# Kernel optimization log

Measured on AMD Instinct MI355X. Metric: run time of the kernel, lower is better.

## Reference

```python
import jax, jax.numpy as jnp
import numpy as np

NUM_HEADS = 16
WINDOW = 256


def setup_inputs() -> dict:
    key = jax.random.key(0)
    ks = jax.random.split(key, 9)
    B, S, E = 2, 2048, 1024
    sc = 1.0 / np.sqrt(E)
    return {
        "x": jax.random.normal(ks[0], (B, S, E), dtype=jnp.float32),
        "Wq": jax.random.normal(ks[1], (E, E), dtype=jnp.float32) * sc,
        "bq": jnp.zeros((E,), dtype=jnp.float32),
        "Wk": jax.random.normal(ks[2], (E, E), dtype=jnp.float32) * sc,
        "bk": jnp.zeros((E,), dtype=jnp.float32),
        "Wv": jax.random.normal(ks[3], (E, E), dtype=jnp.float32) * sc,
        "bv": jnp.zeros((E,), dtype=jnp.float32),
        "Wo": jax.random.normal(ks[4], (E, E), dtype=jnp.float32) * sc,
        "bo": jnp.zeros((E,), dtype=jnp.float32),
    }


def reference(x, Wq, bq, Wk, bk, Wv, bv, Wo, bo):
    B, S, E = x.shape
    H = NUM_HEADS
    D = E // H
    Q = (x @ Wq + bq).reshape(B, S, H, D).transpose(0, 2, 1, 3)  # [B,H,S,D]
    # Faithful to original: K is view(B, H, S, D), NOT a permute of (B,S,H,D)
    K = (x @ Wk + bk).reshape(B, H, S, D)
    V = (x @ Wv + bv).reshape(B, S, H, D).transpose(0, 2, 1, 3)  # [B,H,S,D]
    scores = jnp.einsum('bhqd,bhkd->bhqk', Q, K) / jnp.sqrt(jnp.float32(D))
    # sliding-window mask: j in [i-W, i+W)  (diag included, i+W exclusive)
    i = jnp.arange(S)[:, None]
    j = jnp.arange(S)[None, :]
    mask = (j >= i - WINDOW) & (j < i + WINDOW)  # [S,S]
    scores = jnp.where(mask, scores, -jnp.inf)
    attn = jax.nn.softmax(scores, axis=-1)
    out = jnp.einsum('bhqk,bhkd->bhqd', attn, V)  # [B,H,S,D]
    out = out.transpose(0, 2, 1, 3).reshape(B, S, E)
    return out @ Wo + bo
```

## Files before the change

kernel.cpp:

```cpp
#include <hip/hip_runtime.h>

#define S_LEN 2048
#define EMB   1024
#define HEADS 16
#define HDIM  64
#define WIN   256

typedef unsigned short u16;
typedef unsigned int   u32;
typedef float  f32x4  __attribute__((ext_vector_type(4)));
typedef __bf16 bf16x8 __attribute__((ext_vector_type(8)));
typedef unsigned short u16x4 __attribute__((ext_vector_type(4)));

typedef const __attribute__((address_space(1))) u32* gas_ptr;
typedef __attribute__((address_space(3))) u32*       las_ptr;

__device__ __forceinline__ void gload16(const void* g, void* l) {
    __builtin_amdgcn_global_load_lds((gas_ptr)g, (las_ptr)l, 16, 0, 0);
}

__device__ __forceinline__ u16 f2bf(float v) {
    u32 x = __builtin_bit_cast(u32, v);
    return (u16)((x + 0x7fffu + ((x >> 16) & 1u)) >> 16);
}
__device__ __forceinline__ u32 cvt_pk_bf16(float lo, float hi) {
    u32 r;
    asm volatile("v_cvt_pk_bf16_f32 %0, %1, %2" : "=v"(r) : "v"(lo), "v"(hi));
    return r;
}

__global__ __launch_bounds__(256)
void prep_kernel(const float* __restrict__ W0, const float* __restrict__ W1,
                 const float* __restrict__ W2, const float* __restrict__ W3,
                 u16* __restrict__ T0, u16* __restrict__ T1,
                 u16* __restrict__ T2, u16* __restrict__ T3,
                 const float* __restrict__ x, u16* __restrict__ xh, int n4)
{
    const int z = blockIdx.z;
    const int tid = threadIdx.x;

    if (z == 4) {
        int bid = blockIdx.x + 16 * blockIdx.y;
        for (int i = bid * 256 + tid; i < n4; i += 65536) {
            float4 v = reinterpret_cast<const float4*>(x)[i];
            u16x4 o;
            o[0] = f2bf(v.x); o[1] = f2bf(v.y); o[2] = f2bf(v.z); o[3] = f2bf(v.w);
            reinterpret_cast<u16x4*>(xh)[i] = o;
        }
        return;
    }

    const float* W = (z == 0) ? W0 : (z == 1) ? W1 : (z == 2) ? W2 : W3;
    u16* T = (z == 0) ? T0 : (z == 1) ? T1 : (z == 2) ? T2 : T3;

    __shared__ float Ts[64][68];
    const int k0 = blockIdx.x * 64, n0 = blockIdx.y * 64;

    int r = tid >> 2, c0 = (tid & 3) * 16;
#pragma unroll
    for (int q = 0; q < 4; ++q) {
        float4 v = *reinterpret_cast<const float4*>(W + (size_t)(k0 + r) * EMB + n0 + c0 + 4 * q);
        *reinterpret_cast<float4*>(&Ts[r][c0 + 4 * q]) = v;
    }
    __syncthreads();

    int n = tid >> 2, kk0 = (tid & 3) * 16;
    u16 hb[16];
#pragma unroll
    for (int e = 0; e < 16; ++e) hb[e] = f2bf(Ts[kk0 + e][n]);
    size_t base = (size_t)(n0 + n) * EMB + k0 + kk0;
#pragma unroll
    for (int q = 0; q < 2; ++q) {
        u32 w[4];
#pragma unroll
        for (int e = 0; e < 4; ++e)
            w[e] = (u32)hb[q * 8 + 2 * e] | ((u32)hb[q * 8 + 2 * e + 1] << 16);
        *reinterpret_cast<uint4*>(T + base + q * 8) = make_uint4(w[0], w[1], w[2], w[3]);
    }
}

template<int NFN, bool OUTBF>
__global__ __launch_bounds__(256, 3)
void mfma_gemm(const u16* __restrict__ A,
               const u16* __restrict__ B0, const u16* __restrict__ B1,
               const u16* __restrict__ B2,
               const float* __restrict__ bias0, const float* __restrict__ bias1,
               const float* __restrict__ bias2,
               float s0, float s1, float s2,
               void* __restrict__ Y0, void* __restrict__ Y1, void* __restrict__ Y2,
               int M, int N, int K)
{
    constexpr int TNB = NFN * 32;

    const int z = blockIdx.z;
    const u16*   Bt   = (z == 0) ? B0 : (z == 1) ? B1 : B2;
    const float* bias = (z == 0) ? bias0 : (z == 1) ? bias1 : bias2;
    const float  scl  = (z == 0) ? s0 : (z == 1) ? s1 : s2;
    void*        Y    = (z == 0) ? Y0 : (z == 1) ? Y1 : Y2;

    __shared__ u16 lds[(128 + TNB) * 32];
    u16* lA = lds;
    u16* lB = lds + 128 * 32;

    const int tid  = threadIdx.x;
    const int wid  = tid >> 6, lane = tid & 63;
    const int wr   = wid >> 1, wc = wid & 1;
    const int lr   = lane & 15, lg = lane >> 4;
    const int bm   = blockIdx.y * 128, bn = blockIdx.x * TNB;

    const int srow = lane >> 2;
    const int scol = (lane & 3) * 8;

    f32x4 acc[4][NFN];
#pragma unroll
    for (int i = 0; i < 4; ++i)
#pragma unroll
        for (int j = 0; j < NFN; ++j) acc[i][j] = (f32x4)0.0f;

    for (int k0 = 0; k0 < K; k0 += 32) {
#pragma unroll
        for (int q = 0; q < 2; ++q) {
            int ch = wid + q * 4;
            gload16(A + (size_t)(bm + ch * 16 + srow) * K + k0 + scol,
                    lA + ch * 512);
        }
#pragma unroll
        for (int q = 0; q < TNB / 64; ++q) {
            int ch = wid + q * 4;
            gload16(Bt + (size_t)(bn + ch * 16 + srow) * K + k0 + scol,
                    lB + ch * 512);
        }
        __syncthreads();

        bf16x8 a0[4], b0[NFN];
#pragma unroll
        for (int mf = 0; mf < 4; ++mf)
            a0[mf] = *reinterpret_cast<const bf16x8*>(
                lA + (wr * 64 + mf * 16 + lr) * 32 + lg * 8);
#pragma unroll
        for (int nf = 0; nf < NFN; ++nf)
            b0[nf] = *reinterpret_cast<const bf16x8*>(
                lB + (wc * NFN * 16 + nf * 16 + lr) * 32 + lg * 8);
#pragma unroll
        for (int mf = 0; mf < 4; ++mf)
#pragma unroll
            for (int nf = 0; nf < NFN; ++nf)
                acc[mf][nf] = __builtin_amdgcn_mfma_f32_16x16x32_bf16(
                    a0[mf], b0[nf], acc[mf][nf], 0, 0, 0);
        __syncthreads();
    }

#pragma unroll
    for (int nf = 0; nf < NFN; ++nf) {
        int col = bn + wc * NFN * 16 + nf * 16 + lr;
        float bs = bias[col];
#pragma unroll
        for (int mf = 0; mf < 4; ++mf) {
#pragma unroll
            for (int r = 0; r < 4; ++r) {
                int row = bm + wr * 64 + mf * 16 + lg * 4 + r;
                float val = (acc[mf][nf][r] + bs) * scl;
                if (OUTBF)
                    ((u16*)Y)[(size_t)row * N + col] = f2bf(val);
                else
                    ((float*)Y)[(size_t)row * N + col] = val;
            }
        }
    }
}

__global__ __launch_bounds__(512, 4)
void attn_mfma_kernel(const u16* __restrict__ Qb, const u16* __restrict__ Kb,
                      const u16* __restrict__ Vb, u16* __restrict__ AOh)
{
    __shared__ u16 Ks[64 * 64];
    __shared__ u16 Vt[64 * 64];
    __shared__ u16 Ps[8 * 16 * 64];

    constexpr float L2E = 1.44269504f;

    const int nwg = gridDim.x * gridDim.y * gridDim.z;
    int n  = blockIdx.x + gridDim.x * (blockIdx.y + gridDim.y * blockIdx.z);
    int sw = (n & 7) * (nwg >> 3) + (n >> 3);
    const int qb = sw & 15;
    const int h  = (sw >> 4) & 15;
    const int b  = sw >> 8;

    const int i0  = qb * 128;
    const int tid = threadIdx.x;
    const int wid = tid >> 6, lane = tid & 63;
    const int lr  = lane & 15, lg = lane >> 4;
    const int l7  = lr & 7;

    const u16* Kh = Kb + (size_t)b * S_LEN * EMB + (size_t)h * S_LEN * HDIM;

    bf16x8 qa[2];
    {
        const u16* qp = Qb + ((size_t)(b * S_LEN + i0 + wid * 16 + lr)) * EMB
                        + h * HDIM + lg * 8;
        qa[0] = *reinterpret_cast<const bf16x8*>(qp);
        qa[1] = *reinterpret_cast<const bf16x8*>(qp + 32);
    }

    float m2 = -1e30f, l = 0.0f;
    f32x4 o[4];
#pragma unroll
    for (int nf = 0; nf < 4; ++nf) o[nf] = (f32x4)0.0f;

    const int tlo = (2 * qb < 4) ? 0 : 2 * qb - 4;
    const int thi = (2 * qb + 5 > 31) ? 31 : 2 * qb + 5;
    const int qg  = i0 + wid * 16 + lr;

    const int kj   = lane >> 3;
    const int kgsw = (lane & 7) ^ kj;

    for (int t = tlo; t <= thi; ++t) {
        __syncthreads();

        gload16(Kh + (size_t)(t * 64 + wid * 8 + kj) * HDIM + kgsw * 8,
                Ks + wid * 512);

        {
            int jp = (tid & 31) * 2, dc = tid >> 5;
            const u16* vp = Vb + ((size_t)(b * S_LEN + t * 64 + jp)) * EMB
                            + h * HDIM + dc * 4;
            uint2 r0 = *reinterpret_cast<const uint2*>(vp);
            uint2 r1 = *reinterpret_cast<const uint2*>(vp + EMB);
            const u16* e0 = reinterpret_cast<const u16*>(&r0);
            const u16* e1 = reinterpret_cast<const u16*>(&r1);
            int jg = jp >> 3, jl = jp & 7;
#pragma unroll
            for (int e = 0; e < 4; ++e) {
                int d = dc * 4 + e;
                u32 w = (u32)e0[e] | ((u32)e1[e] << 16);
                *reinterpret_cast<u32*>(Vt + d * 64 + ((jg ^ (d & 7)) << 3) + jl) = w;
            }
        }
        __syncthreads();

        f32x4 s[4];
#pragma unroll
        for (int nf = 0; nf < 4; ++nf) s[nf] = (f32x4)0.0f;
#pragma unroll
        for (int ks = 0; ks < 2; ++ks) {
            int cg = (ks * 4 + lg) ^ l7;
#pragma unroll
            for (int nf = 0; nf < 4; ++nf) {
                bf16x8 kf = *reinterpret_cast<const bf16x8*>(
                    Ks + (nf * 16 + lr) * 64 + (cg << 3));
                s[nf] = __builtin_amdgcn_mfma_f32_16x16x32_bf16(kf, qa[ks], s[nf], 0, 0, 0);
            }
        }

        if (t <= 2 * qb - 3 || t >= 2 * qb + 4) {
            int klo = qg - WIN, khi = qg + WIN;
#pragma unroll
            for (int nf = 0; nf < 4; ++nf) {
#pragma unroll
                for (int r = 0; r < 4; ++r) {
                    int kg = t * 64 + nf * 16 + lg * 4 + r;
                    bool ok = (kg >= klo) && (kg < khi);
                    s[nf][r] = ok ? s[nf][r] : -1e30f;
                }
            }
        }

        float tmax = s[0][0];
#pragma unroll
        for (int nf = 0; nf < 4; ++nf)
#pragma unroll
            for (int r = 0; r < 4; ++r) tmax = fmaxf(tmax, s[nf][r]);
        tmax = fmaxf(tmax, __shfl_xor(tmax, 16));
        tmax = fmaxf(tmax, __shfl_xor(tmax, 32));
        float tmax2 = tmax * L2E;

        bool need = tmax2 > m2 + 12.0f;
        if (__any(need)) {
            float mn2 = fmaxf(m2, tmax2);
            float sc = __builtin_amdgcn_exp2f(m2 - mn2);
            m2 = mn2;
            l *= sc;
#pragma unroll
            for (int r = 0; r < 4; ++r) {
                float scr = __shfl(sc, lg * 4 + r);
#pragma unroll
                for (int nf = 0; nf < 4; ++nf) o[nf][r] *= scr;
            }
        }

        float ps = 0.0f;
#pragma unroll
        for (int nf = 0; nf < 4; ++nf) {
            float p0 = __builtin_amdgcn_exp2f(fmaf(s[nf][0], L2E, -m2));
            float p1 = __builtin_amdgcn_exp2f(fmaf(s[nf][1], L2E, -m2));
            float p2 = __builtin_amdgcn_exp2f(fmaf(s[nf][2], L2E, -m2));
            float p3 = __builtin_amdgcn_exp2f(fmaf(s[nf][3], L2E, -m2));
            ps += (p0 + p1) + (p2 + p3);
            u32 pk0 = cvt_pk_bf16(p0, p1);
            u32 pk1 = cvt_pk_bf16(p2, p3);
            int idx16 = wid * 1024 + lr * 64 +
                        (((nf * 2 + (lg >> 1)) ^ l7) << 3) + (lg & 1) * 4;
            *reinterpret_cast<uint2*>(Ps + idx16) = make_uint2(pk0, pk1);
        }
        ps += __shfl_xor(ps, 16);
        ps += __shfl_xor(ps, 32);
        l += ps;

#pragma unroll
        for (int ks = 0; ks < 2; ++ks) {
            int cg = (ks * 4 + lg) ^ l7;
            bf16x8 pf = *reinterpret_cast<const bf16x8*>(
                Ps + wid * 1024 + lr * 64 + (cg << 3));
#pragma unroll
            for (int nf = 0; nf < 4; ++nf) {
                bf16x8 vf = *reinterpret_cast<const bf16x8*>(
                    Vt + (nf * 16 + lr) * 64 + (cg << 3));
                o[nf] = __builtin_amdgcn_mfma_f32_16x16x32_bf16(pf, vf, o[nf], 0, 0, 0);
            }
        }
    }

    float inv = 1.0f / l;
#pragma unroll
    for (int r = 0; r < 4; ++r) {
        float invr = __shfl(inv, lg * 4 + r);
#pragma unroll
        for (int nf = 0; nf < 4; ++nf) {
            size_t idx = ((size_t)(b * S_LEN + i0 + wid * 16 + lg * 4 + r)) * EMB
                         + h * HDIM + nf * 16 + lr;
            AOh[idx] = f2bf(o[nf][r] * invr);
        }
    }
}

extern "C" void kernel_launch(void* const* d_in, const int* in_sizes, int n_in,
                              void* d_out, int out_size, void* d_ws, size_t ws_size,
                              hipStream_t stream)
{
    (void)n_in; (void)out_size; (void)ws_size;
    const float* x  = (const float*)d_in[0];
    const float* Wq = (const float*)d_in[1];
    const float* bq = (const float*)d_in[2];
    const float* Wk = (const float*)d_in[3];
    const float* bk = (const float*)d_in[4];
    const float* Wv = (const float*)d_in[5];
    const float* bv = (const float*)d_in[6];
    const float* Wo = (const float*)d_in[7];
    const float* bo = (const float*)d_in[8];
    float* out = (float*)d_out;

    const int B = in_sizes[0] / (S_LEN * EMB);
    const int M = B * S_LEN;

    u16* xh  = (u16*)d_ws;
    u16* WtQ = xh  + (size_t)M * EMB;
    u16* WtK = WtQ + (size_t)EMB * EMB;
    u16* WtV = WtK + (size_t)EMB * EMB;
    u16* WtO = WtV + (size_t)EMB * EMB;
    u16* Qb  = WtO + (size_t)EMB * EMB;
    u16* Kb  = Qb + (size_t)M * EMB;
    u16* Vb  = Kb + (size_t)M * EMB;
    u16* AOh = Vb + (size_t)M * EMB;

    int n4 = M * EMB / 4;
    dim3 gt(EMB / 64, EMB / 64, 5);
    prep_kernel<<<gt, 256, 0, stream>>>(Wq, Wk, Wv, Wo, WtQ, WtK, WtV, WtO,
                                        x, xh, n4);

    dim3 g1(EMB / 128, M / 128, 3);
    mfma_gemm<4, true><<<g1, 256, 0, stream>>>(
        xh, WtQ, WtK, WtV, bq, bk, bv, 0.125f, 1.0f, 1.0f,
        Qb, Kb, Vb, M, EMB, EMB);

    dim3 g2(S_LEN / 128, HEADS, B);
    attn_mfma_kernel<<<g2, 512, 0, stream>>>(Qb, Kb, Vb, AOh);

    dim3 g3(EMB / 64, M / 128, 1);
    mfma_gemm<2, false><<<g3, 256, 0, stream>>>(
        AOh, WtO, WtO, WtO, bo, bo, bo, 1.0f, 1.0f, 1.0f,
        out, out, out, M, EMB, EMB);
}
```

Measured before the change: 93.49 us.

## Double-buffer attention K/V tiles and deepen GEMM K-step with swizzled LDS

The attention kernel now keeps two LDS buffers for K and V. It prefetches the next tile's K (async global-to-LDS) and V (into registers) while computing on the current tile, which cuts the barriers per iteration from two to one and hides global load latency. The projection GEMM moves from a K-step of 32 to 64, using an XOR-swizzled LDS layout so the wider rows are read without bank conflicts. This halves the loop iterations and barriers. In exchange, LDS use in both kernels roughly doubles, which may reduce occupancy, and more registers are held across the iteration.

```diff
diff --git a/kernel.cpp b/kernel.cpp
--- a/kernel.cpp
+++ b/kernel.cpp
@@ -98,18 +98,19 @@
     const float  scl  = (z == 0) ? s0 : (z == 1) ? s1 : s2;
     void*        Y    = (z == 0) ? Y0 : (z == 1) ? Y1 : Y2;
 
-    __shared__ u16 lds[(128 + TNB) * 32];
+    __shared__ u16 lds[(128 + TNB) * 64];
     u16* lA = lds;
-    u16* lB = lds + 128 * 32;
+    u16* lB = lds + 128 * 64;
 
     const int tid  = threadIdx.x;
     const int wid  = tid >> 6, lane = tid & 63;
     const int wr   = wid >> 1, wc = wid & 1;
     const int lr   = lane & 15, lg = lane >> 4;
+    const int l7   = lr & 7;
     const int bm   = blockIdx.y * 128, bn = blockIdx.x * TNB;
 
-    const int srow = lane >> 2;
-    const int scol = (lane & 3) * 8;
+    const int crow = lane >> 3;
+    const int cgrp = (lane & 7) ^ crow;
 
     f32x4 acc[4][NFN];
 #pragma unroll
@@ -117,36 +118,40 @@
 #pragma unroll
         for (int j = 0; j < NFN; ++j) acc[i][j] = (f32x4)0.0f;
 
-    for (int k0 = 0; k0 < K; k0 += 32) {
-#pragma unroll
-        for (int q = 0; q < 2; ++q) {
-            int ch = wid + q * 4;
-            gload16(A + (size_t)(bm + ch * 16 + srow) * K + k0 + scol,
+    for (int k0 = 0; k0 < K; k0 += 64) {
+#pragma unroll
+        for (int q = 0; q < 4; ++q) {
+            int ch = wid * 4 + q;
+            gload16(A + (size_t)(bm + ch * 8 + crow) * K + k0 + cgrp * 8,
                     lA + ch * 512);
         }
 #pragma unroll
-        for (int q = 0; q < TNB / 64; ++q) {
-            int ch = wid + q * 4;
-            gload16(Bt + (size_t)(bn + ch * 16 + srow) * K + k0 + scol,
+        for (int q = 0; q < TNB / 32; ++q) {
+            int ch = wid * (TNB / 32) + q;
+            gload16(Bt + (size_t)(bn + ch * 8 + crow) * K + k0 + cgrp * 8,
                     lB + ch * 512);
         }
         __syncthreads();
 
-        bf16x8 a0[4], b0[NFN];
-#pragma unroll
-        for (int mf = 0; mf < 4; ++mf)
-            a0[mf] = *reinterpret_cast<const bf16x8*>(
-                lA + (wr * 64 + mf * 16 + lr) * 32 + lg * 8);
-#pragma unroll
-        for (int nf = 0; nf < NFN; ++nf)
-            b0[nf] = *reinterpret_cast<const bf16x8*>(
-                lB + (wc * NFN * 16 + nf * 16 + lr) * 32 + lg * 8);
-#pragma unroll
-        for (int mf = 0; mf < 4; ++mf)
+#pragma unroll
+        for (int ks = 0; ks < 2; ++ks) {
+            const int gsw = ((ks * 4 + lg) ^ l7) << 3;
+            bf16x8 a0[4], b0[NFN];
+#pragma unroll
+            for (int mf = 0; mf < 4; ++mf)
+                a0[mf] = *reinterpret_cast<const bf16x8*>(
+                    lA + (wr * 64 + mf * 16 + lr) * 64 + gsw);
 #pragma unroll
             for (int nf = 0; nf < NFN; ++nf)
-                acc[mf][nf] = __builtin_amdgcn_mfma_f32_16x16x32_bf16(
-                    a0[mf], b0[nf], acc[mf][nf], 0, 0, 0);
+                b0[nf] = *reinterpret_cast<const bf16x8*>(
+                    lB + (wc * NFN * 16 + nf * 16 + lr) * 64 + gsw);
+#pragma unroll
+            for (int mf = 0; mf < 4; ++mf)
+#pragma unroll
+                for (int nf = 0; nf < NFN; ++nf)
+                    acc[mf][nf] = __builtin_amdgcn_mfma_f32_16x16x32_bf16(
+                        a0[mf], b0[nf], acc[mf][nf], 0, 0, 0);
+        }
         __syncthreads();
     }
 
@@ -173,8 +178,8 @@
 void attn_mfma_kernel(const u16* __restrict__ Qb, const u16* __restrict__ Kb,
                       const u16* __restrict__ Vb, u16* __restrict__ AOh)
 {
-    __shared__ u16 Ks[64 * 64];
-    __shared__ u16 Vt[64 * 64];
+    __shared__ u16 Ks[2][64 * 64];
+    __shared__ u16 Vt[2][64 * 64];
     __shared__ u16 Ps[8 * 16 * 64];
 
     constexpr float L2E = 1.44269504f;
@@ -214,29 +219,35 @@
     const int kj   = lane >> 3;
     const int kgsw = (lane & 7) ^ kj;
 
+    const int vjp = (tid & 31) * 2, vdc = tid >> 5;
+    const u16* Vh = Vb + (size_t)b * S_LEN * EMB + h * HDIM;
+
+    uint2 vr0 = *reinterpret_cast<const uint2*>(Vh + (size_t)(tlo * 64 + vjp) * EMB + vdc * 4);
+    uint2 vr1 = *reinterpret_cast<const uint2*>(Vh + (size_t)(tlo * 64 + vjp + 1) * EMB + vdc * 4);
+    gload16(Kh + (size_t)(tlo * 64 + wid * 8 + kj) * HDIM + kgsw * 8,
+            Ks[0] + wid * 512);
+
+    int cur = 0;
     for (int t = tlo; t <= thi; ++t) {
+        {
+            const u16* e0 = reinterpret_cast<const u16*>(&vr0);
+            const u16* e1 = reinterpret_cast<const u16*>(&vr1);
+            int jg = vjp >> 3, jl = vjp & 7;
+#pragma unroll
+            for (int e = 0; e < 4; ++e) {
+                int d = vdc * 4 + e;
+                u32 w = (u32)e0[e] | ((u32)e1[e] << 16);
+                *reinterpret_cast<u32*>(Vt[cur] + d * 64 + ((jg ^ (d & 7)) << 3) + jl) = w;
+            }
+        }
         __syncthreads();
 
-        gload16(Kh + (size_t)(t * 64 + wid * 8 + kj) * HDIM + kgsw * 8,
-                Ks + wid * 512);
-
-        {
-            int jp = (tid & 31) * 2, dc = tid >> 5;
-            const u16* vp = Vb + ((size_t)(b * S_LEN + t * 64 + jp)) * EMB
-                            + h * HDIM + dc * 4;
-            uint2 r0 = *reinterpret_cast<const uint2*>(vp);
-            uint2 r1 = *reinterpret_cast<const uint2*>(vp + EMB);
-            const u16* e0 = reinterpret_cast<const u16*>(&r0);
-            const u16* e1 = reinterpret_cast<const u16*>(&r1);
-            int jg = jp >> 3, jl = jp & 7;
-#pragma unroll
-            for (int e = 0; e < 4; ++e) {
-                int d = dc * 4 + e;
-                u32 w = (u32)e0[e] | ((u32)e1[e] << 16);
-                *reinterpret_cast<u32*>(Vt + d * 64 + ((jg ^ (d & 7)) << 3) + jl) = w;
-            }
-        }
-        __syncthreads();
+        if (t < thi) {
+            gload16(Kh + (size_t)((t + 1) * 64 + wid * 8 + kj) * HDIM + kgsw * 8,
+                    Ks[cur ^ 1] + wid * 512);
+            vr0 = *reinterpret_cast<const uint2*>(Vh + (size_t)((t + 1) * 64 + vjp) * EMB + vdc * 4);
+            vr1 = *reinterpret_cast<const uint2*>(Vh + (size_t)((t + 1) * 64 + vjp + 1) * EMB + vdc * 4);
+        }
 
         f32x4 s[4];
 #pragma unroll
@@ -247,7 +258,7 @@
 #pragma unroll
             for (int nf = 0; nf < 4; ++nf) {
                 bf16x8 kf = *reinterpret_cast<const bf16x8*>(
-                    Ks + (nf * 16 + lr) * 64 + (cg << 3));
+                    Ks[cur] + (nf * 16 + lr) * 64 + (cg << 3));
                 s[nf] = __builtin_amdgcn_mfma_f32_16x16x32_bf16(kf, qa[ks], s[nf], 0, 0, 0);
             }
         }
@@ -314,10 +325,11 @@
 #pragma unroll
             for (int nf = 0; nf < 4; ++nf) {
                 bf16x8 vf = *reinterpret_cast<const bf16x8*>(
-                    Vt + (nf * 16 + lr) * 64 + (cg << 3));
+                    Vt[cur] + (nf * 16 + lr) * 64 + (cg << 3));
                 o[nf] = __builtin_amdgcn_mfma_f32_16x16x32_bf16(pf, vf, o[nf], 0, 0, 0);
             }
         }
+        cur ^= 1;
     }
 
     float inv = 1.0f / l;
```

New measurement: 87.77 us. -6.1%, faster.
